# Kernel tuning notes

Measured on AMD Instinct MI355X. Metric: run time of the kernel, lower is better.

The kernel has to match this reference:

```python
import jax, jax.numpy as jnp
import numpy as np

N, E, FE = 20000, 160000, 500000
IN, HC, HEADS = 128, 64, 4
HEADC = HC // HEADS          # 16
DV = HEADC                   # 16
KHOP = 3
NUM_T = 128
OUT = 1
CST = 1e-5


def _lin(key, fan_in, fan_out):
    kw, kb = jax.random.split(key)
    s = 1.0 / np.sqrt(fan_in)
    W = jax.random.uniform(kw, (fan_in, fan_out), minval=-s, maxval=s, dtype=jnp.float32)
    b = jax.random.uniform(kb, (fan_out,), minval=-s, maxval=s, dtype=jnp.float32)
    return W, b


def setup_inputs() -> dict:
    key = jax.random.key(0)
    ks = jax.random.split(key, 16)
    x = jax.random.normal(ks[0], (N, IN), dtype=jnp.float32)
    edge_index = jax.random.randint(ks[1], (2, E), 0, N, dtype=jnp.int32)
    full_edge_index = jax.random.randint(ks[2], (2, FE), 0, N, dtype=jnp.int32)
    time_steps = jax.random.randint(ks[3], (N,), 0, NUM_T, dtype=jnp.int32)
    Wi, bi = _lin(ks[4], IN, HC)
    Wt1, bt1 = _lin(ks[5], HC, 4 * HC)
    Wt2, bt2 = _lin(ks[6], 4 * HC, HC)
    WQ, bQ = _lin(ks[7], HC, HEADS * HEADC)
    WK, bK = _lin(ks[8], HC, HEADS * HEADC)
    WV, bV = _lin(ks[9], HC, HEADS * DV)
    Wo, bo = _lin(ks[10], HEADS * DV, DV)
    hopwise = jnp.ones((KHOP + 1,), dtype=jnp.float32)
    headwise = jnp.zeros((HEADS, KHOP), dtype=jnp.float32)
    Wf1, bf1 = _lin(ks[11], 2 * DV, DV)
    Wf2, bf2 = _lin(ks[12], DV, OUT)
    return dict(x=x, edge_index=edge_index, full_edge_index=full_edge_index,
                time_steps=time_steps, Wi=Wi, bi=bi, Wt1=Wt1, bt1=bt1,
                Wt2=Wt2, bt2=bt2, WQ=WQ, bQ=bQ, WK=WK, bK=bK, WV=WV, bV=bV,
                Wo=Wo, bo=bo, hopwise=hopwise, headwise=headwise,
                Wf1=Wf1, bf1=bf1, Wf2=Wf2, bf2=bf2)


def _sin_emb(t, dim, num_steps, rescale=4000.0):
    # Sinusoidal timestep embedding rescaled by num_steps (diffusion style).
    t = t.astype(jnp.float32) * (rescale / num_steps)
    half = dim // 2
    freqs = jnp.exp(-jnp.log(10000.0) / (half - 1) * jnp.arange(half, dtype=jnp.float32))
    args = t[:, None] * freqs[None, :]
    return jnp.concatenate([jnp.sin(args), jnp.cos(args)], axis=-1)


def reference(x, edge_index, full_edge_index, time_steps,
              Wi, bi, Wt1, bt1, Wt2, bt2, WQ, bQ, WK, bK, WV, bV,
              Wo, bo, hopwise, headwise, Wf1, bf1, Wf2, bf2):
    n = x.shape[0]
    row, col = edge_index[0], edge_index[1]

    # random-walk norm: deg over destination (col), norm gathered at source (row)
    deg = jax.ops.segment_sum(jnp.ones_like(col, dtype=x.dtype), col, num_segments=n)
    deg_inv = jnp.where(deg > 0, 1.0 / deg, 0.0)
    norm = deg_inv[row]                                   # [E]

    t_emb = _sin_emb(time_steps, HC, NUM_T)               # [N, HC]
    t_emb = jax.nn.silu(t_emb @ Wt1 + bt1) @ Wt2 + bt2    # [N, HC]

    h = jax.nn.relu(x @ Wi + bi + t_emb)                  # [N, HC]

    Q = (1.0 + jax.nn.elu(h @ WQ + bQ)).reshape(n, HEADS, HEADC)
    Kf = (1.0 + jax.nn.elu(h @ WK + bK)).reshape(n, HEADS, HEADC)
    V = (h @ WV + bV).reshape(n, HEADS, DV)

    M = jnp.einsum('nhi,nhj->nhij', Kf, V)                # [N, H, hc, dv]
    hidden = V * hopwise[0]
    layerwise = jax.nn.softmax(headwise, axis=0)          # softmax over heads

    for hop in range(KHOP):
        # gather-scale-scatter message passing (random walk propagation)
        M = jax.ops.segment_sum(M[row] * norm[:, None, None, None], col, num_segments=n)
        Kf = jax.ops.segment_sum(Kf[row] * norm[:, None, None], col, num_segments=n)
        H = jnp.einsum('nhi,nhij->nhj', Q, M)             # [N, H, dv]
        C = jnp.einsum('nhi,nhi->nh', Q, Kf)[..., None] + CST
        gamma = hopwise[hop + 1] * layerwise[:, hop][:, None]   # [H, 1]
        hidden = hidden + gamma * (H / C)

    # multi_concat output projection
    hidden = hidden.reshape(n, HEADS * DV) @ Wo + bo      # [N, DV]

    src, dst = full_edge_index[0], full_edge_index[1]
    he = jnp.concatenate([hidden[src], hidden[dst]], axis=-1)  # [FE, 2*DV]
    edge_logits = jax.nn.silu(he @ Wf1 + bf1) @ Wf2 + bf2      # [FE, OUT]
    return edge_logits, hidden
```

## Files before the change

### kernel.cpp

```cpp
#include <hip/hip_runtime.h>
#include <math.h>


#define HC 64
#define HEADS 4
#define KHOP 3
#define NUM_T 128
#define MSZ 1024
#define SLOTS 64
#define CST 1e-5f

typedef float f32x2 __attribute__((ext_vector_type(2)));

__device__ __forceinline__ float bf2f(unsigned short s) { return __uint_as_float(((unsigned int)s) << 16); }
__device__ __forceinline__ float bfu_lo(unsigned int u) { return __uint_as_float(u << 16); }
__device__ __forceinline__ float bfu_hi(unsigned int u) { return __uint_as_float(u & 0xffff0000u); }
__device__ __forceinline__ unsigned short f2bf(float f) {
    unsigned int u = __float_as_uint(f);
    u = (u + 0x7fffu + ((u >> 16) & 1u)) >> 16;
    return (unsigned short)u;
}
__device__ __forceinline__ unsigned int pack4fp8(float a, float b, float c, float d) {
    int r = __builtin_amdgcn_cvt_pk_fp8_f32(a, b, 0, false);
    r = __builtin_amdgcn_cvt_pk_fp8_f32(c, d, r, true);
    return (unsigned int)r;
}

__global__ void k_fill(const int* __restrict__ row, const int* __restrict__ col,
                       int* __restrict__ cnt, int* __restrict__ csr, int E) {
    int e = blockIdx.x * 256 + threadIdx.x;
    if (e >= E) return;
    int c = col[e];
    int r = row[e];
    int k = atomicAdd(&cnt[c], 1);
    if (k < SLOTS) csr[c * SLOTS + k] = r;
}

__global__ __launch_bounds__(256) void k_misc(
    const float* __restrict__ Wt1, const float* __restrict__ bt1,
    const float* __restrict__ Wt2, const float* __restrict__ bt2,
    const float* __restrict__ hopwise, const float* __restrict__ headwise,
    const int* __restrict__ cnt,
    float* __restrict__ gamma, float* __restrict__ table,
    float* __restrict__ inv_deg, int n) {
    if (blockIdx.x >= NUM_T) {
        int i = (blockIdx.x - NUM_T) * 256 + threadIdx.x;
        if (i < n) {
            int d = cnt[i];
            inv_deg[i] = (d > 0) ? 1.0f / (float)min(d, SLOTS) : 0.0f;
        }
        return;
    }
    if (blockIdx.x == 0 && threadIdx.x == 0) {
        for (int k = 0; k < KHOP; k++) {
            float m = -1e30f;
            for (int h2 = 0; h2 < HEADS; h2++) m = fmaxf(m, headwise[h2 * KHOP + k]);
            float ex[HEADS]; float s = 0.f;
            for (int h2 = 0; h2 < HEADS; h2++) { ex[h2] = expf(headwise[h2 * KHOP + k] - m); s += ex[h2]; }
            for (int h2 = 0; h2 < HEADS; h2++) gamma[k * HEADS + h2] = hopwise[k + 1] * ex[h2] / s;
        }
    }
    int t = threadIdx.x;
    int tval = blockIdx.x;
    __shared__ float emb_s[64];
    __shared__ float z1_s[256];
    __shared__ float ps_s[4][64];
    if (t < 64) {
        float tt = (float)tval * 31.25f;
        float e;
        if (t < 32) e = sinf(tt * expf(-0.2971077539347156f * (float)t));
        else        e = cosf(tt * expf(-0.2971077539347156f * (float)(t - 32)));
        emb_s[t] = e;
    }
    __syncthreads();
    {
        float acc = bt1[t];
        #pragma unroll 8
        for (int i = 0; i < 64; i++) acc += emb_s[i] * Wt1[i * 256 + t];
        z1_s[t] = acc / (1.f + expf(-acc));
    }
    __syncthreads();
    {
        int j = t & 63, p = t >> 6;
        float acc = 0.f;
        #pragma unroll 8
        for (int i = 0; i < 64; i++) acc += z1_s[p * 64 + i] * Wt2[(p * 64 + i) * 64 + j];
        ps_s[p][j] = acc;
    }
    __syncthreads();
    if (t < 64)
        table[tval * 64 + t] = ps_s[0][t] + ps_s[1][t] + ps_s[2][t] + ps_s[3][t] + bt2[t];
}

__global__ __launch_bounds__(256) void k_node(
    const float* __restrict__ x, const int* __restrict__ time_steps,
    const float* __restrict__ temb, const float* __restrict__ Wi,
    const float* __restrict__ bi,
    const float* __restrict__ WQ, const float* __restrict__ bQ,
    const float* __restrict__ WK, const float* __restrict__ bK,
    const float* __restrict__ WV, const float* __restrict__ bV,
    const float* __restrict__ hopwise, const float* __restrict__ inv_deg,
    float* __restrict__ Q, unsigned short* __restrict__ Kf0,
    unsigned short* __restrict__ Vbuf, float* __restrict__ hidden, int n) {
    __shared__ float xs[16][128];
    __shared__ float hs[16][64];
    int j = threadIdx.x & 63;
    int slot = threadIdx.x >> 6;
    int nbase = blockIdx.x * 16;
    int nvalid = min(16, n - nbase);
    const float4* xg = (const float4*)(x + (size_t)nbase * 128);
    float4* xs4 = (float4*)&xs[0][0];
    for (int idx = threadIdx.x; idx < nvalid * 32; idx += 256) xs4[idx] = xg[idx];
    __syncthreads();
    int nl = slot * 4;
    {
        float acc[4];
        #pragma unroll
        for (int k = 0; k < 4; k++) acc[k] = 0.f;
        #pragma unroll 8
        for (int i = 0; i < 128; i++) {
            float w = Wi[i * 64 + j];
            #pragma unroll
            for (int k = 0; k < 4; k++) acc[k] += xs[nl + k][i] * w;
        }
        float bj = bi[j];
        #pragma unroll
        for (int k = 0; k < 4; k++) {
            int node = nbase + nl + k;
            float te = (node < n) ? temb[time_steps[node] * 64 + j] : 0.f;
            hs[nl + k][j] = fmaxf(acc[k] + bj + te, 0.f);
        }
    }
    __syncthreads();
    float aq[4], ak[4], av[4];
    #pragma unroll
    for (int k = 0; k < 4; k++) { aq[k] = bQ[j]; ak[k] = bK[j]; av[k] = bV[j]; }
    #pragma unroll 4
    for (int i = 0; i < 64; i++) {
        float wq = WQ[i * 64 + j], wk = WK[i * 64 + j], wv = WV[i * 64 + j];
        #pragma unroll
        for (int k = 0; k < 4; k++) {
            float hv = hs[nl + k][i];
            aq[k] += hv * wq; ak[k] += hv * wk; av[k] += hv * wv;
        }
    }
    float h0 = hopwise[0];
    #pragma unroll
    for (int k = 0; k < 4; k++) {
        int node = nbase + nl + k;
        if (node < n) {
            float q  = 1.f + ((aq[k] > 0.f) ? aq[k] : (expf(aq[k]) - 1.f));
            float kf = 1.f + ((ak[k] > 0.f) ? ak[k] : (expf(ak[k]) - 1.f));
            float inv = inv_deg[node];
            Q[(size_t)node * 64 + j] = q;
            Kf0[(size_t)node * 64 + j] = f2bf(kf * inv);
            Vbuf[(size_t)node * 64 + j] = f2bf(av[k]);
            hidden[(size_t)node * 64 + j] = av[k] * h0;
        }
    }
}

template<int MODE>
__global__ __launch_bounds__(128) void k_hop(
    const unsigned char* __restrict__ Mold, const unsigned short* __restrict__ Kfold,
    const unsigned short* __restrict__ Vbuf,
    const int* __restrict__ cnt, const int* __restrict__ csr,
    const float* __restrict__ inv_deg, const float* __restrict__ Q,
    const float* __restrict__ gamma,
    unsigned char* __restrict__ Mnew, unsigned short* __restrict__ Kfnew,
    float* __restrict__ hidden, int hop, int write_out,
    const float* __restrict__ Wo, const float* __restrict__ bo,
    const float* __restrict__ Wf1, float* __restrict__ out16,
    float* __restrict__ Pbuf, int n) {
    constexpr int DEPTH = (MODE == 0) ? 4 : 8;
    int lane = threadIdx.x & 63;
    int node = blockIdx.x * 2 + (threadIdx.x >> 6);
    if (node >= n) return;
    int grp = lane >> 4;
    int deg = min(cnt[node], SLOTS);
    int sidx = csr[(size_t)node * SLOTS + lane];
    float qv = Q[(size_t)node * 64 + lane];
    size_t hoff = (size_t)node * 64 + lane;
    float hid_in = hidden[hoff];
    int degU = __builtin_amdgcn_readfirstlane(deg);
    float acc[16];
    #pragma unroll
    for (int t = 0; t < 16; t++) acc[t] = 0.f;
    float kacc = 0.f;

    int d = 0;
    for (; d + DEPTH <= degU; d += DEPTH) {
        unsigned short kraw[DEPTH];
        uint4 m0[DEPTH], m1[DEPTH];
        #pragma unroll
        for (int t = 0; t < DEPTH; t++) {
            int s = __builtin_amdgcn_readlane(sidx, d + t);
            kraw[t] = Kfold[(size_t)s * 64 + lane];
            if constexpr (MODE == 0) {
                const uint4* vp = (const uint4*)((const unsigned char*)Vbuf + (size_t)s * 128 + grp * 32);
                m0[t] = vp[0]; m1[t] = vp[1];
            } else {
                m0[t] = *(const uint4*)(Mold + (size_t)s * MSZ + lane * 16);
            }
        }
        #pragma unroll
        for (int t = 0; t < DEPTH; t++) {
            float kf = bf2f(kraw[t]);
            kacc += kf;
            if constexpr (MODE == 0) {
                acc[0]  = fmaf(kf, bfu_lo(m0[t].x), acc[0]);
                acc[1]  = fmaf(kf, bfu_hi(m0[t].x), acc[1]);
                acc[2]  = fmaf(kf, bfu_lo(m0[t].y), acc[2]);
                acc[3]  = fmaf(kf, bfu_hi(m0[t].y), acc[3]);
                acc[4]  = fmaf(kf, bfu_lo(m0[t].z), acc[4]);
                acc[5]  = fmaf(kf, bfu_hi(m0[t].z), acc[5]);
                acc[6]  = fmaf(kf, bfu_lo(m0[t].w), acc[6]);
                acc[7]  = fmaf(kf, bfu_hi(m0[t].w), acc[7]);
                acc[8]  = fmaf(kf, bfu_lo(m1[t].x), acc[8]);
                acc[9]  = fmaf(kf, bfu_hi(m1[t].x), acc[9]);
                acc[10] = fmaf(kf, bfu_lo(m1[t].y), acc[10]);
                acc[11] = fmaf(kf, bfu_hi(m1[t].y), acc[11]);
                acc[12] = fmaf(kf, bfu_lo(m1[t].z), acc[12]);
                acc[13] = fmaf(kf, bfu_hi(m1[t].z), acc[13]);
                acc[14] = fmaf(kf, bfu_lo(m1[t].w), acc[14]);
                acc[15] = fmaf(kf, bfu_hi(m1[t].w), acc[15]);
            } else {
                f32x2 p;
                p = __builtin_amdgcn_cvt_pk_f32_fp8((int)m0[t].x, false); acc[0]  += p.x; acc[1]  += p.y;
                p = __builtin_amdgcn_cvt_pk_f32_fp8((int)m0[t].x, true);  acc[2]  += p.x; acc[3]  += p.y;
                p = __builtin_amdgcn_cvt_pk_f32_fp8((int)m0[t].y, false); acc[4]  += p.x; acc[5]  += p.y;
                p = __builtin_amdgcn_cvt_pk_f32_fp8((int)m0[t].y, true);  acc[6]  += p.x; acc[7]  += p.y;
                p = __builtin_amdgcn_cvt_pk_f32_fp8((int)m0[t].z, false); acc[8]  += p.x; acc[9]  += p.y;
                p = __builtin_amdgcn_cvt_pk_f32_fp8((int)m0[t].z, true);  acc[10] += p.x; acc[11] += p.y;
                p = __builtin_amdgcn_cvt_pk_f32_fp8((int)m0[t].w, false); acc[12] += p.x; acc[13] += p.y;
                p = __builtin_amdgcn_cvt_pk_f32_fp8((int)m0[t].w, true);  acc[14] += p.x; acc[15] += p.y;
            }
        }
    }
    if (d < degU) {
        int rem = degU - d;
        unsigned short kraw[DEPTH];
        uint4 m0[DEPTH], m1[DEPTH];
        #pragma unroll
        for (int t = 0; t < DEPTH - 1; t++) {
            if (t < rem) {
                int s = __builtin_amdgcn_readlane(sidx, d + t);
                kraw[t] = Kfold[(size_t)s * 64 + lane];
                if constexpr (MODE == 0) {
                    const uint4* vp = (const uint4*)((const unsigned char*)Vbuf + (size_t)s * 128 + grp * 32);
                    m0[t] = vp[0]; m1[t] = vp[1];
                } else {
                    m0[t] = *(const uint4*)(Mold + (size_t)s * MSZ + lane * 16);
                }
            }
        }
        #pragma unroll
        for (int t = 0; t < DEPTH - 1; t++) {
            if (t < rem) {
                float kf = bf2f(kraw[t]);
                kacc += kf;
                if constexpr (MODE == 0) {
                    acc[0]  = fmaf(kf, bfu_lo(m0[t].x), acc[0]);
                    acc[1]  = fmaf(kf, bfu_hi(m0[t].x), acc[1]);
                    acc[2]  = fmaf(kf, bfu_lo(m0[t].y), acc[2]);
                    acc[3]  = fmaf(kf, bfu_hi(m0[t].y), acc[3]);
                    acc[4]  = fmaf(kf, bfu_lo(m0[t].z), acc[4]);
                    acc[5]  = fmaf(kf, bfu_hi(m0[t].z), acc[5]);
                    acc[6]  = fmaf(kf, bfu_lo(m0[t].w), acc[6]);
                    acc[7]  = fmaf(kf, bfu_hi(m0[t].w), acc[7]);
                    acc[8]  = fmaf(kf, bfu_lo(m1[t].x), acc[8]);
                    acc[9]  = fmaf(kf, bfu_hi(m1[t].x), acc[9]);
                    acc[10] = fmaf(kf, bfu_lo(m1[t].y), acc[10]);
                    acc[11] = fmaf(kf, bfu_hi(m1[t].y), acc[11]);
                    acc[12] = fmaf(kf, bfu_lo(m1[t].z), acc[12]);
                    acc[13] = fmaf(kf, bfu_hi(m1[t].z), acc[13]);
                    acc[14] = fmaf(kf, bfu_lo(m1[t].w), acc[14]);
                    acc[15] = fmaf(kf, bfu_hi(m1[t].w), acc[15]);
                } else {
                    f32x2 p;
                    p = __builtin_amdgcn_cvt_pk_f32_fp8((int)m0[t].x, false); acc[0]  += p.x; acc[1]  += p.y;
                    p = __builtin_amdgcn_cvt_pk_f32_fp8((int)m0[t].x, true);  acc[2]  += p.x; acc[3]  += p.y;
                    p = __builtin_amdgcn_cvt_pk_f32_fp8((int)m0[t].y, false); acc[4]  += p.x; acc[5]  += p.y;
                    p = __builtin_amdgcn_cvt_pk_f32_fp8((int)m0[t].y, true);  acc[6]  += p.x; acc[7]  += p.y;
                    p = __builtin_amdgcn_cvt_pk_f32_fp8((int)m0[t].z, false); acc[8]  += p.x; acc[9]  += p.y;
                    p = __builtin_amdgcn_cvt_pk_f32_fp8((int)m0[t].z, true);  acc[10] += p.x; acc[11] += p.y;
                    p = __builtin_amdgcn_cvt_pk_f32_fp8((int)m0[t].w, false); acc[12] += p.x; acc[13] += p.y;
                    p = __builtin_amdgcn_cvt_pk_f32_fp8((int)m0[t].w, true);  acc[14] += p.x; acc[15] += p.y;
                }
            }
        }
    }

    if (write_out) {
        float inv = inv_deg[node];
        uint4 st;
        st.x = pack4fp8(acc[0] * inv,  acc[1] * inv,  acc[2] * inv,  acc[3] * inv);
        st.y = pack4fp8(acc[4] * inv,  acc[5] * inv,  acc[6] * inv,  acc[7] * inv);
        st.z = pack4fp8(acc[8] * inv,  acc[9] * inv,  acc[10] * inv, acc[11] * inv);
        st.w = pack4fp8(acc[12] * inv, acc[13] * inv, acc[14] * inv, acc[15] * inv);
        *(uint4*)(Mnew + (size_t)node * MSZ + lane * 16) = st;
        Kfnew[(size_t)node * 64 + lane] = f2bf(kacc * inv);
    }

    float c = qv * kacc;
    c += __shfl_xor(c, 1); c += __shfl_xor(c, 2); c += __shfl_xor(c, 4); c += __shfl_xor(c, 8);

    float w0[16];
    #pragma unroll
    for (int t = 0; t < 16; t++) w0[t] = qv * acc[t];
    float w1r[8];
    #pragma unroll
    for (int t = 0; t < 8; t++) {
        float a = w0[2 * t], b = w0[2 * t + 1];
        float mine = (lane & 1) ? b : a, th = (lane & 1) ? a : b;
        w1r[t] = mine + __shfl_xor(th, 1);
    }
    float w2r[4];
    #pragma unroll
    for (int t = 0; t < 4; t++) {
        float a = w1r[2 * t], b = w1r[2 * t + 1];
        float mine = (lane & 2) ? b : a, th = (lane & 2) ? a : b;
        w2r[t] = mine + __shfl_xor(th, 2);
    }
    float w3r[2];
    #pragma unroll
    for (int t = 0; t < 2; t++) {
        float a = w2r[2 * t], b = w2r[2 * t + 1];
        float mine = (lane & 4) ? b : a, th = (lane & 4) ? a : b;
        w3r[t] = mine + __shfl_xor(th, 4);
    }
    float Hv;
    {
        float a = w3r[0], b = w3r[1];
        float mine = (lane & 8) ? b : a, th = (lane & 8) ? a : b;
        Hv = mine + __shfl_xor(th, 8);
    }

    float g = gamma[hop * HEADS + grp];
    float contrib = g * Hv / (c + CST);
    if (write_out) {
        hidden[hoff] = hid_in + contrib;
    } else {
        float hid = hid_in + contrib;
        const float4* wop = (const float4*)(Wo + lane * 16);
        float4 wo0 = wop[0], wo1 = wop[1], wo2 = wop[2], wo3 = wop[3];
        float v[16];
        v[0] = hid * wo0.x;  v[1] = hid * wo0.y;  v[2] = hid * wo0.z;  v[3] = hid * wo0.w;
        v[4] = hid * wo1.x;  v[5] = hid * wo1.y;  v[6] = hid * wo1.z;  v[7] = hid * wo1.w;
        v[8] = hid * wo2.x;  v[9] = hid * wo2.y;  v[10] = hid * wo2.z; v[11] = hid * wo2.w;
        v[12] = hid * wo3.x; v[13] = hid * wo3.y; v[14] = hid * wo3.z; v[15] = hid * wo3.w;
        #pragma unroll
        for (int m = 32; m >= 1; m >>= 1) {
            #pragma unroll
            for (int o = 0; o < 16; o++) v[o] += __shfl_xor(v[o], m);
        }
        #pragma unroll
        for (int o = 0; o < 16; o++) v[o] += bo[o];
        if (lane == 0) {
            float4* op = (float4*)(out16 + (size_t)node * 16);
            op[0] = make_float4(v[0],  v[1],  v[2],  v[3]);
            op[1] = make_float4(v[4],  v[5],  v[6],  v[7]);
            op[2] = make_float4(v[8],  v[9],  v[10], v[11]);
            op[3] = make_float4(v[12], v[13], v[14], v[15]);
        }
        if (lane < 32) {
            int o = lane & 15, half = lane >> 4;
            const float* wf = Wf1 + (size_t)(half * 16) * 16 + o;
            float p = 0.f;
            #pragma unroll
            for (int i = 0; i < 16; i++) p += v[i] * wf[i * 16];
            Pbuf[(size_t)node * 32 + lane] = p;
        }
    }
}

__global__ __launch_bounds__(256) void k_edge(
    const int* __restrict__ src, const int* __restrict__ dst,
    const float* __restrict__ Pbuf,
    const float* __restrict__ bf1, const float* __restrict__ Wf2,
    const float* __restrict__ bf2,
    float* __restrict__ out, int fe) {
    __shared__ float b1[16];
    __shared__ float w2[16];
    __shared__ float b2s;
    int t = threadIdx.x;
    if (t < 16) { b1[t] = bf1[t]; w2[t] = Wf2[t]; }
    if (t == 0) b2s = bf2[0];
    __syncthreads();
    int e = blockIdx.x * 256 + t;
    if (e >= fe) return;
    int s = src[e], d = dst[e];
    const float4* p1 = (const float4*)(Pbuf + (size_t)s * 32);
    const float4* p2 = (const float4*)(Pbuf + (size_t)d * 32 + 16);
    float z[16];
    #pragma unroll
    for (int q = 0; q < 4; q++) {
        float4 a = p1[q]; float4 b = p2[q];
        z[q * 4 + 0] = a.x + b.x; z[q * 4 + 1] = a.y + b.y;
        z[q * 4 + 2] = a.z + b.z; z[q * 4 + 3] = a.w + b.w;
    }
    float acc = b2s;
    #pragma unroll
    for (int o = 0; o < 16; o++) {
        float zz = z[o] + b1[o];
        zz = zz / (1.f + expf(-zz));
// ... 17 lines not shown
    const float* bt2 = (const float*)d_in[9];
    const float* WQ  = (const float*)d_in[10];
    const float* bQ  = (const float*)d_in[11];
    const float* WK  = (const float*)d_in[12];
    const float* bK  = (const float*)d_in[13];
    const float* WV  = (const float*)d_in[14];
    const float* bV  = (const float*)d_in[15];
    const float* Wo  = (const float*)d_in[16];
    const float* bo  = (const float*)d_in[17];
    const float* hopwise  = (const float*)d_in[18];
    const float* headwise = (const float*)d_in[19];
    const float* Wf1 = (const float*)d_in[20];
    const float* bf1 = (const float*)d_in[21];
    const float* Wf2 = (const float*)d_in[22];
    const float* bf2 = (const float*)d_in[23];

    const int N  = in_sizes[3];
    const int E  = in_sizes[1] / 2;
    const int FE = in_sizes[2] / 2;
    const int* row = eidx;
    const int* col = eidx + E;
    const int* fsrc = feidx;
    const int* fdst = feidx + FE;

    char* ws = (char*)d_ws;
    size_t off = 0;
    auto alloc = [&](size_t bytes) -> char* {
        char* p = ws + off;
        off = (off + bytes + 255) & ~(size_t)255;
        return p;
    };
    float* gamma     = (float*)alloc(KHOP * HEADS * sizeof(float));
    int*   cnt       = (int*)alloc((size_t)N * 4);
    int*   csr       = (int*)alloc((size_t)N * SLOTS * 4);
    float* inv_deg   = (float*)alloc((size_t)N * 4);
    float* temb      = (float*)alloc((size_t)NUM_T * HC * 4);
    float* Qbuf      = (float*)alloc((size_t)N * HC * 4);
    unsigned short* Kf0  = (unsigned short*)alloc((size_t)N * HC * 2);
    unsigned short* Kf_a = (unsigned short*)alloc((size_t)N * HC * 2);
    unsigned short* Kf_b = (unsigned short*)alloc((size_t)N * HC * 2);
    unsigned short* Vbuf = (unsigned short*)alloc((size_t)N * HC * 2);
    float* hidden    = (float*)alloc((size_t)N * HC * 4);
    unsigned char* M_a = (unsigned char*)alloc((size_t)N * MSZ);
    unsigned char* M_b = (unsigned char*)alloc((size_t)N * MSZ);
    float* Pbuf      = (float*)alloc((size_t)N * 32 * 4);
    (void)ws_size;

    float* out_edges = (float*)d_out;
    float* out_hid16 = (float*)d_out + FE;

    const int miscBlocks = NUM_T + (N + 255) / 256;
    const int hopBlocks = (N + 1) / 2;

    (void)hipMemsetAsync(cnt, 0, (size_t)N * 4, stream);
    k_fill<<<(E + 255) / 256, 256, 0, stream>>>(row, col, cnt, csr, E);
    k_misc<<<miscBlocks, 256, 0, stream>>>(Wt1, bt1, Wt2, bt2, hopwise, headwise,
                                           cnt, gamma, temb, inv_deg, N);
    k_node<<<(N + 15) / 16, 256, 0, stream>>>(x, tsteps, temb, Wi, bi,
                                              WQ, bQ, WK, bK, WV, bV, hopwise, inv_deg,
                                              Qbuf, Kf0, Vbuf, hidden, N);
    k_hop<0><<<hopBlocks, 128, 0, stream>>>(nullptr, Kf0, Vbuf, cnt, csr, inv_deg, Qbuf, gamma,
                                            M_a, Kf_a, hidden, 0, 1, Wo, bo, Wf1, out_hid16, Pbuf, N);
    k_hop<1><<<hopBlocks, 128, 0, stream>>>(M_a, Kf_a, nullptr, cnt, csr, inv_deg, Qbuf, gamma,
                                            M_b, Kf_b, hidden, 1, 1, Wo, bo, Wf1, out_hid16, Pbuf, N);
    k_hop<1><<<hopBlocks, 128, 0, stream>>>(M_b, Kf_b, nullptr, cnt, csr, inv_deg, Qbuf, gamma,
                                            M_a, Kf_a, hidden, 2, 0, Wo, bo, Wf1, out_hid16, Pbuf, N);
    k_edge<<<(FE + 255) / 256, 256, 0, stream>>>(fsrc, fdst, Pbuf, bf1, Wf2, bf2,
                                                 out_edges, FE);
}
```

Baseline: 253.9 us.

## Split hop kernel across 8 M-slices per node group and defer combine to new kernel

Result: slower. 351.9 us (+38.6%).

```diff
diff --git a/kernel.cpp b/kernel.cpp
--- a/kernel.cpp
+++ b/kernel.cpp
@@ -99,9 +99,9 @@
     const float* __restrict__ WQ, const float* __restrict__ bQ,
     const float* __restrict__ WK, const float* __restrict__ bK,
     const float* __restrict__ WV, const float* __restrict__ bV,
-    const float* __restrict__ hopwise, const float* __restrict__ inv_deg,
+    const float* __restrict__ inv_deg,
     float* __restrict__ Q, unsigned short* __restrict__ Kf0,
-    unsigned short* __restrict__ Vbuf, float* __restrict__ hidden, int n) {
+    unsigned short* __restrict__ Vbuf, int n) {
     __shared__ float xs[16][128];
     __shared__ float hs[16][64];
     int j = threadIdx.x & 63;
@@ -144,7 +144,6 @@
             aq[k] += hv * wq; ak[k] += hv * wk; av[k] += hv * wv;
         }
     }
-    float h0 = hopwise[0];
     #pragma unroll
     for (int k = 0; k < 4; k++) {
         int node = nbase + nl + k;
@@ -155,222 +154,173 @@
             Q[(size_t)node * 64 + j] = q;
             Kf0[(size_t)node * 64 + j] = f2bf(kf * inv);
             Vbuf[(size_t)node * 64 + j] = f2bf(av[k]);
-            hidden[(size_t)node * 64 + j] = av[k] * h0;
         }
     }
 }
 
 template<int MODE>
-__global__ __launch_bounds__(128) void k_hop(
+__global__ __launch_bounds__(256) void k_hop(
     const unsigned char* __restrict__ Mold, const unsigned short* __restrict__ Kfold,
-    const unsigned short* __restrict__ Vbuf,
+    const unsigned short* __restrict__ Vb,
     const int* __restrict__ cnt, const int* __restrict__ csr,
     const float* __restrict__ inv_deg, const float* __restrict__ Q,
-    const float* __restrict__ gamma,
     unsigned char* __restrict__ Mnew, unsigned short* __restrict__ Kfnew,
-    float* __restrict__ hidden, int hop, int write_out,
-    const float* __restrict__ Wo, const float* __restrict__ bo,
-    const float* __restrict__ Wf1, float* __restrict__ out16,
-    float* __restrict__ Pbuf, int n) {
-    constexpr int DEPTH = (MODE == 0) ? 4 : 8;
+    float* __restrict__ Hp, float* __restrict__ Cp,
+    int hop, int write_out, int n) {
     int lane = threadIdx.x & 63;
-    int node = blockIdx.x * 2 + (threadIdx.x >> 6);
-    if (node >= n) return;
-    int grp = lane >> 4;
-    int deg = min(cnt[node], SLOTS);
-    int sidx = csr[(size_t)node * SLOTS + lane];
-    float qv = Q[(size_t)node * 64 + lane];
-    size_t hoff = (size_t)node * 64 + lane;
-    float hid_in = hidden[hoff];
-    int degU = __builtin_amdgcn_readfirstlane(deg);
-    float acc[16];
-    #pragma unroll
-    for (int t = 0; t < 16; t++) acc[t] = 0.f;
+    int wv   = threadIdx.x >> 6;
+    int slice = blockIdx.x & 7;
+    int ngrp  = blockIdx.x >> 3;
+    int ell   = lane & 15;
+    int gbase = lane & 48;
+    int node  = ngrp * 16 + wv * 4 + (lane >> 4);
+    int h = slice >> 1, ib = (slice & 1) * 8;
+    int i_loc = ell >> 1, jh = ell & 1;
+    bool valid = node < n;
+    int deg = 0; int s0 = 0, s1 = 0, s2 = 0, s3 = 0; float qv = 0.f;
+    if (valid) {
+        deg = min(__builtin_nontemporal_load(cnt + node), SLOTS);
+        const int* cb = csr + (size_t)node * SLOTS;
+        s0 = __builtin_nontemporal_load(cb + ell);
+        s1 = __builtin_nontemporal_load(cb + 16 + ell);
+        s2 = __builtin_nontemporal_load(cb + 32 + ell);
+        s3 = __builtin_nontemporal_load(cb + 48 + ell);
+        qv = Q[(size_t)node * 64 + h * 16 + ib + i_loc];
+    }
+    int dm = max(deg, __shfl_xor(deg, 16));
+    dm = max(dm, __shfl_xor(dm, 32));
+    int degU = __builtin_amdgcn_readfirstlane(dm);
+
+    float acc[8];
+    #pragma unroll
+    for (int t = 0; t < 8; t++) acc[t] = 0.f;
     float kacc = 0.f;
 
-    int d = 0;
-    for (; d + DEPTH <= degU; d += DEPTH) {
-        unsigned short kraw[DEPTH];
-        uint4 m0[DEPTH], m1[DEPTH];
-        #pragma unroll
-        for (int t = 0; t < DEPTH; t++) {
-            int s = __builtin_amdgcn_readlane(sidx, d + t);
-            kraw[t] = Kfold[(size_t)s * 64 + lane];
-            if constexpr (MODE == 0) {
-                const uint4* vp = (const uint4*)((const unsigned char*)Vbuf + (size_t)s * 128 + grp * 32);
-                m0[t] = vp[0]; m1[t] = vp[1];
-            } else {
-                m0[t] = *(const uint4*)(Mold + (size_t)s * MSZ + lane * 16);
-            }
-        }
-        #pragma unroll
-        for (int t = 0; t < DEPTH; t++) {
-            float kf = bf2f(kraw[t]);
-            kacc += kf;
-            if constexpr (MODE == 0) {
-                acc[0]  = fmaf(kf, bfu_lo(m0[t].x), acc[0]);
-                acc[1]  = fmaf(kf, bfu_hi(m0[t].x), acc[1]);
-                acc[2]  = fmaf(kf, bfu_lo(m0[t].y), acc[2]);
-                acc[3]  = fmaf(kf, bfu_hi(m0[t].y), acc[3]);
-                acc[4]  = fmaf(kf, bfu_lo(m0[t].z), acc[4]);
-                acc[5]  = fmaf(kf, bfu_hi(m0[t].z), acc[5]);
-                acc[6]  = fmaf(kf, bfu_lo(m0[t].w), acc[6]);
-                acc[7]  = fmaf(kf, bfu_hi(m0[t].w), acc[7]);
-                acc[8]  = fmaf(kf, bfu_lo(m1[t].x), acc[8]);
-                acc[9]  = fmaf(kf, bfu_hi(m1[t].x), acc[9]);
-                acc[10] = fmaf(kf, bfu_lo(m1[t].y), acc[10]);
-                acc[11] = fmaf(kf, bfu_hi(m1[t].y), acc[11]);
-                acc[12] = fmaf(kf, bfu_lo(m1[t].z), acc[12]);
-                acc[13] = fmaf(kf, bfu_hi(m1[t].z), acc[13]);
-                acc[14] = fmaf(kf, bfu_lo(m1[t].w), acc[14]);
-                acc[15] = fmaf(kf, bfu_hi(m1[t].w), acc[15]);
-            } else {
-                f32x2 p;
-                p = __builtin_amdgcn_cvt_pk_f32_fp8((int)m0[t].x, false); acc[0]  += p.x; acc[1]  += p.y;
-                p = __builtin_amdgcn_cvt_pk_f32_fp8((int)m0[t].x, true);  acc[2]  += p.x; acc[3]  += p.y;
-                p = __builtin_amdgcn_cvt_pk_f32_fp8((int)m0[t].y, false); acc[4]  += p.x; acc[5]  += p.y;
-                p = __builtin_amdgcn_cvt_pk_f32_fp8((int)m0[t].y, true);  acc[6]  += p.x; acc[7]  += p.y;
-                p = __builtin_amdgcn_cvt_pk_f32_fp8((int)m0[t].z, false); acc[8]  += p.x; acc[9]  += p.y;
-                p = __builtin_amdgcn_cvt_pk_f32_fp8((int)m0[t].z, true);  acc[10] += p.x; acc[11] += p.y;
-                p = __builtin_amdgcn_cvt_pk_f32_fp8((int)m0[t].w, false); acc[12] += p.x; acc[13] += p.y;
-                p = __builtin_amdgcn_cvt_pk_f32_fp8((int)m0[t].w, true);  acc[14] += p.x; acc[15] += p.y;
-            }
-        }
-    }
-    if (d < degU) {
-        int rem = degU - d;
-        unsigned short kraw[DEPTH];
-        uint4 m0[DEPTH], m1[DEPTH];
-        #pragma unroll
-        for (int t = 0; t < DEPTH - 1; t++) {
-            if (t < rem) {
-                int s = __builtin_amdgcn_readlane(sidx, d + t);
-                kraw[t] = Kfold[(size_t)s * 64 + lane];
-                if constexpr (MODE == 0) {
-                    const uint4* vp = (const uint4*)((const unsigned char*)Vbuf + (size_t)s * 128 + grp * 32);
-                    m0[t] = vp[0]; m1[t] = vp[1];
-                } else {
-                    m0[t] = *(const uint4*)(Mold + (size_t)s * MSZ + lane * 16);
+    constexpr int SUB = (MODE == 0) ? 8 : 16;
+    #pragma unroll
+    for (int blk = 0; blk < 4; blk++) {
+        if (blk * 16 >= degU) break;
+        int sreg = (blk == 0) ? s0 : (blk == 1) ? s1 : (blk == 2) ? s2 : s3;
+        #pragma unroll
+        for (int sb = 0; sb < 16 / SUB; sb++) {
+            unsigned int kr[SUB];
+            uint2 mv[(MODE == 1) ? SUB : 1];
+            uint4 vvv[(MODE == 0) ? SUB : 1];
+            #pragma unroll
+            for (int t = 0; t < SUB; t++) {
+                int sl = sb * SUB + t;
+                int q = blk * 16 + sl;
+                int sv = __shfl(sreg, gbase + sl);
+                kr[t] = 0u;
+                if constexpr (MODE == 0) { vvv[t] = make_uint4(0, 0, 0, 0); }
+                else { mv[t].x = 0u; mv[t].y = 0u; }
+                if (q < deg) {
+                    kr[t] = (unsigned int)Kfold[(size_t)sv * 64 + h * 16 + ib + i_loc];
+                    if constexpr (MODE == 0)
+                        vvv[t] = *(const uint4*)(Vb + (size_t)sv * 64 + h * 16 + jh * 8);
+                    else
+                        mv[t] = *(const uint2*)(Mold + (size_t)sv * MSZ + slice * 128 + ell * 8);
                 }
             }
-        }
-        #pragma unroll
-        for (int t = 0; t < DEPTH - 1; t++) {
-            if (t < rem) {
-                float kf = bf2f(kraw[t]);
+            #pragma unroll
+            for (int t = 0; t < SUB; t++) {
+                float kf = bf2f((unsigned short)kr[t]);
                 kacc += kf;
                 if constexpr (MODE == 0) {
-                    acc[0]  = fmaf(kf, bfu_lo(m0[t].x), acc[0]);
-                    acc[1]  = fmaf(kf, bfu_hi(m0[t].x), acc[1]);
-                    acc[2]  = fmaf(kf, bfu_lo(m0[t].y), acc[2]);
-                    acc[3]  = fmaf(kf, bfu_hi(m0[t].y), acc[3]);
-                    acc[4]  = fmaf(kf, bfu_lo(m0[t].z), acc[4]);
-                    acc[5]  = fmaf(kf, bfu_hi(m0[t].z), acc[5]);
-                    acc[6]  = fmaf(kf, bfu_lo(m0[t].w), acc[6]);
-                    acc[7]  = fmaf(kf, bfu_hi(m0[t].w), acc[7]);
-                    acc[8]  = fmaf(kf, bfu_lo(m1[t].x), acc[8]);
-                    acc[9]  = fmaf(kf, bfu_hi(m1[t].x), acc[9]);
-                    acc[10] = fmaf(kf, bfu_lo(m1[t].y), acc[10]);
-                    acc[11] = fmaf(kf, bfu_hi(m1[t].y), acc[11]);
-                    acc[12] = fmaf(kf, bfu_lo(m1[t].z), acc[12]);
-                    acc[13] = fmaf(kf, bfu_hi(m1[t].z), acc[13]);
-                    acc[14] = fmaf(kf, bfu_lo(m1[t].w), acc[14]);
-                    acc[15] = fmaf(kf, bfu_hi(m1[t].w), acc[15]);
+                    acc[0] += kf * bfu_lo(vvv[t].x); acc[1] += kf * bfu_hi(vvv[t].x);
+                    acc[2] += kf * bfu_lo(vvv[t].y); acc[3] += kf * bfu_hi(vvv[t].y);
+                    acc[4] += kf * bfu_lo(vvv[t].z); acc[5] += kf * bfu_hi(vvv[t].z);
+                    acc[6] += kf * bfu_lo(vvv[t].w); acc[7] += kf * bfu_hi(vvv[t].w);
                 } else {
                     f32x2 p;
-                    p = __builtin_amdgcn_cvt_pk_f32_fp8((int)m0[t].x, false); acc[0]  += p.x; acc[1]  += p.y;
-                    p = __builtin_amdgcn_cvt_pk_f32_fp8((int)m0[t].x, true);  acc[2]  += p.x; acc[3]  += p.y;
-                    p = __builtin_amdgcn_cvt_pk_f32_fp8((int)m0[t].y, false); acc[4]  += p.x; acc[5]  += p.y;
-                    p = __builtin_amdgcn_cvt_pk_f32_fp8((int)m0[t].y, true);  acc[6]  += p.x; acc[7]  += p.y;
-                    p = __builtin_amdgcn_cvt_pk_f32_fp8((int)m0[t].z, false); acc[8]  += p.x; acc[9]  += p.y;
-                    p = __builtin_amdgcn_cvt_pk_f32_fp8((int)m0[t].z, true);  acc[10] += p.x; acc[11] += p.y;
-                    p = __builtin_amdgcn_cvt_pk_f32_fp8((int)m0[t].w, false); acc[12] += p.x; acc[13] += p.y;
-                    p = __builtin_amdgcn_cvt_pk_f32_fp8((int)m0[t].w, true);  acc[14] += p.x; acc[15] += p.y;
+                    p = __builtin_amdgcn_cvt_pk_f32_fp8((int)mv[t].x, false); acc[0] += p.x; acc[1] += p.y;
+                    p = __builtin_amdgcn_cvt_pk_f32_fp8((int)mv[t].x, true);  acc[2] += p.x; acc[3] += p.y;
+                    p = __builtin_amdgcn_cvt_pk_f32_fp8((int)mv[t].y, false); acc[4] += p.x; acc[5] += p.y;
+                    p = __builtin_amdgcn_cvt_pk_f32_fp8((int)mv[t].y, true);  acc[6] += p.x; acc[7] += p.y;
                 }
             }
         }
     }
 
-    if (write_out) {
+    if (valid && write_out) {
         float inv = inv_deg[node];
-        uint4 st;
-        st.x = pack4fp8(acc[0] * inv,  acc[1] * inv,  acc[2] * inv,  acc[3] * inv);
-        st.y = pack4fp8(acc[4] * inv,  acc[5] * inv,  acc[6] * inv,  acc[7] * inv);
-        st.z = pack4fp8(acc[8] * inv,  acc[9] * inv,  acc[10] * inv, acc[11] * inv);
-        st.w = pack4fp8(acc[12] * inv, acc[13] * inv, acc[14] * inv, acc[15] * inv);
-        *(uint4*)(Mnew + (size_t)node * MSZ + lane * 16) = st;
-        Kfnew[(size_t)node * 64 + lane] = f2bf(kacc * inv);
-    }
-
-    float c = qv * kacc;
-    c += __shfl_xor(c, 1); c += __shfl_xor(c, 2); c += __shfl_xor(c, 4); c += __shfl_xor(c, 8);
-
-    float w0[16];
-    #pragma unroll
-    for (int t = 0; t < 16; t++) w0[t] = qv * acc[t];
-    float w1r[8];
-    #pragma unroll
-    for (int t = 0; t < 8; t++) {
-        float a = w0[2 * t], b = w0[2 * t + 1];
-        float mine = (lane & 1) ? b : a, th = (lane & 1) ? a : b;
-        w1r[t] = mine + __shfl_xor(th, 1);
-    }
-    float w2r[4];
-    #pragma unroll
-    for (int t = 0; t < 4; t++) {
-        float a = w1r[2 * t], b = w1r[2 * t + 1];
-        float mine = (lane & 2) ? b : a, th = (lane & 2) ? a : b;
-        w2r[t] = mine + __shfl_xor(th, 2);
-    }
-    float w3r[2];
-    #pragma unroll
-    for (int t = 0; t < 2; t++) {
-        float a = w2r[2 * t], b = w2r[2 * t + 1];
-        float mine = (lane & 4) ? b : a, th = (lane & 4) ? a : b;
-        w3r[t] = mine + __shfl_xor(th, 4);
-    }
-    float Hv;
-    {
-        float a = w3r[0], b = w3r[1];
-        float mine = (lane & 8) ? b : a, th = (lane & 8) ? a : b;
-        Hv = mine + __shfl_xor(th, 8);
-    }
-
-    float g = gamma[hop * HEADS + grp];
-    float contrib = g * Hv / (c + CST);
-    if (write_out) {
-        hidden[hoff] = hid_in + contrib;
-    } else {
-        float hid = hid_in + contrib;
-        const float4* wop = (const float4*)(Wo + lane * 16);
-        float4 wo0 = wop[0], wo1 = wop[1], wo2 = wop[2], wo3 = wop[3];
-        float v[16];
-        v[0] = hid * wo0.x;  v[1] = hid * wo0.y;  v[2] = hid * wo0.z;  v[3] = hid * wo0.w;
-        v[4] = hid * wo1.x;  v[5] = hid * wo1.y;  v[6] = hid * wo1.z;  v[7] = hid * wo1.w;
-        v[8] = hid * wo2.x;  v[9] = hid * wo2.y;  v[10] = hid * wo2.z; v[11] = hid * wo2.w;
-        v[12] = hid * wo3.x; v[13] = hid * wo3.y; v[14] = hid * wo3.z; v[15] = hid * wo3.w;
-        #pragma unroll
-        for (int m = 32; m >= 1; m >>= 1) {
-            #pragma unroll
-            for (int o = 0; o < 16; o++) v[o] += __shfl_xor(v[o], m);
-        }
-        #pragma unroll
-        for (int o = 0; o < 16; o++) v[o] += bo[o];
-        if (lane == 0) {
-            float4* op = (float4*)(out16 + (size_t)node * 16);
-            op[0] = make_float4(v[0],  v[1],  v[2],  v[3]);
-            op[1] = make_float4(v[4],  v[5],  v[6],  v[7]);
-            op[2] = make_float4(v[8],  v[9],  v[10], v[11]);
-            op[3] = make_float4(v[12], v[13], v[14], v[15]);
-        }
-        if (lane < 32) {
-            int o = lane & 15, half = lane >> 4;
-            const float* wf = Wf1 + (size_t)(half * 16) * 16 + o;
-            float p = 0.f;
-            #pragma unroll
-            for (int i = 0; i < 16; i++) p += v[i] * wf[i * 16];
-            Pbuf[(size_t)node * 32 + lane] = p;
-        }
+        uint2 st;
+        st.x = pack4fp8(acc[0] * inv, acc[1] * inv, acc[2] * inv, acc[3] * inv);
+        st.y = pack4fp8(acc[4] * inv, acc[5] * inv, acc[6] * inv, acc[7] * inv);
+        *(uint2*)(Mnew + (size_t)node * MSZ + slice * 128 + ell * 8) = st;
+        if (jh == 0) Kfnew[(size_t)node * 64 + h * 16 + ib + i_loc] = f2bf(kacc * inv);
+    }
+
+    float w[8];
+    #pragma unroll
+    for (int k = 0; k < 8; k++) w[k] = qv * acc[k];
+    #pragma unroll
+    for (int m = 2; m <= 8; m <<= 1) {
+        #pragma unroll
+        for (int k = 0; k < 8; k++) w[k] += __shfl_xor(w[k], m);
+    }
+    float ck = (jh == 0) ? qv * kacc : 0.f;
+    ck += __shfl_xor(ck, 1); ck += __shfl_xor(ck, 2);
+    ck += __shfl_xor(ck, 4); ck += __shfl_xor(ck, 8);
+
+    if (valid) {
+        float* hpb = Hp + ((size_t)hop * n + node) * 128 + slice * 16;
+        if (ell < 2) {
+            *(float4*)(hpb + jh * 8)     = make_float4(w[0], w[1], w[2], w[3]);
+            *(float4*)(hpb + jh * 8 + 4) = make_float4(w[4], w[5], w[6], w[7]);
+        }
+        if (ell == 0) Cp[((size_t)hop * n + node) * 8 + slice] = ck;
+    }
+}
+
+__global__ __launch_bounds__(256) void k_comb(
+    const unsigned short* __restrict__ Vb,
+    const float* __restrict__ Hp, const float* __restrict__ Cp,
+    const float* __restrict__ gamma, const float* __restrict__ hopwise,
+    const float* __restrict__ Wo, const float* __restrict__ bo,
+    const float* __restrict__ Wf1,
+    float* __restrict__ out16, float* __restrict__ Pbuf, int n) {
+    int lane = threadIdx.x & 63;
+    int node = blockIdx.x * 4 + (threadIdx.x >> 6);
+    if (node >= n) return;
+    int h = lane >> 4, j = lane & 15;
+    float hid = hopwise[0] * bf2f(Vb[(size_t)node * 64 + lane]);
+    #pragma unroll
+    for (int hop = 0; hop < KHOP; hop++) {
+        const float* hpb = Hp + ((size_t)hop * n + node) * 128;
+        const float* cpb = Cp + ((size_t)hop * n + node) * 8;
+        float Hs = hpb[(2 * h) * 16 + j] + hpb[(2 * h + 1) * 16 + j];
+        float Cs = cpb[2 * h] + cpb[2 * h + 1] + CST;
+        hid += gamma[hop * HEADS + h] * Hs / Cs;
+    }
+    const float4* wop = (const float4*)(Wo + lane * 16);
+    float4 wo0 = wop[0], wo1 = wop[1], wo2 = wop[2], wo3 = wop[3];
+    float v[16];
+    v[0] = hid * wo0.x;  v[1] = hid * wo0.y;  v[2] = hid * wo0.z;  v[3] = hid * wo0.w;
+    v[4] = hid * wo1.x;  v[5] = hid * wo1.y;  v[6] = hid * wo1.z;  v[7] = hid * wo1.w;
+    v[8] = hid * wo2.x;  v[9] = hid * wo2.y;  v[10] = hid * wo2.z; v[11] = hid * wo2.w;
+    v[12] = hid * wo3.x; v[13] = hid * wo3.y; v[14] = hid * wo3.z; v[15] = hid * wo3.w;
+    #pragma unroll
+    for (int m = 32; m >= 1; m >>= 1) {
+        #pragma unroll
+        for (int o = 0; o < 16; o++) v[o] += __shfl_xor(v[o], m);
+    }
+    #pragma unroll
+    for (int o = 0; o < 16; o++) v[o] += bo[o];
+    if (lane == 0) {
+        float4* op = (float4*)(out16 + (size_t)node * 16);
+        op[0] = make_float4(v[0],  v[1],  v[2],  v[3]);
+        op[1] = make_float4(v[4],  v[5],  v[6],  v[7]);
+        op[2] = make_float4(v[8],  v[9],  v[10], v[11]);
+        op[3] = make_float4(v[12], v[13], v[14], v[15]);
+    }
+    if (lane < 32) {
+        int o = lane & 15, half = lane >> 4;
+        const float* wf = Wf1 + (size_t)(half * 16) * 16 + o;
+        float p = 0.f;
+        #pragma unroll
+        for (int i = 0; i < 16; i++) p += v[i] * wf[i * 16];
+        Pbuf[(size_t)node * 32 + lane] = p;
     }
 }
 
@@ -462,9 +412,10 @@
     unsigned short* Kf_a = (unsigned short*)alloc((size_t)N * HC * 2);
     unsigned short* Kf_b = (unsigned short*)alloc((size_t)N * HC * 2);
     unsigned short* Vbuf = (unsigned short*)alloc((size_t)N * HC * 2);
-    float* hidden    = (float*)alloc((size_t)N * HC * 4);
     unsigned char* M_a = (unsigned char*)alloc((size_t)N * MSZ);
     unsigned char* M_b = (unsigned char*)alloc((size_t)N * MSZ);
+    float* Hp        = (float*)alloc((size_t)KHOP * N * 128 * 4);
+    float* Cp        = (float*)alloc((size_t)KHOP * N * 8 * 4);
     float* Pbuf      = (float*)alloc((size_t)N * 32 * 4);
     (void)ws_size;
 
@@ -472,21 +423,23 @@
     float* out_hid16 = (float*)d_out + FE;
 
     const int miscBlocks = NUM_T + (N + 255) / 256;
-    const int hopBlocks = (N + 1) / 2;
+    const int hopBlocks = 8 * ((N + 15) / 16);
 
     (void)hipMemsetAsync(cnt, 0, (size_t)N * 4, stream);
     k_fill<<<(E + 255) / 256, 256, 0, stream>>>(row, col, cnt, csr, E);
     k_misc<<<miscBlocks, 256, 0, stream>>>(Wt1, bt1, Wt2, bt2, hopwise, headwise,
                                            cnt, gamma, temb, inv_deg, N);
     k_node<<<(N + 15) / 16, 256, 0, stream>>>(x, tsteps, temb, Wi, bi,
-                                              WQ, bQ, WK, bK, WV, bV, hopwise, inv_deg,
-                                              Qbuf, Kf0, Vbuf, hidden, N);
-    k_hop<0><<<hopBlocks, 128, 0, stream>>>(nullptr, Kf0, Vbuf, cnt, csr, inv_deg, Qbuf, gamma,
-                                            M_a, Kf_a, hidden, 0, 1, Wo, bo, Wf1, out_hid16, Pbuf, N);
-    k_hop<1><<<hopBlocks, 128, 0, stream>>>(M_a, Kf_a, nullptr, cnt, csr, inv_deg, Qbuf, gamma,
-                                            M_b, Kf_b, hidden, 1, 1, Wo, bo, Wf1, out_hid16, Pbuf, N);
-    k_hop<1><<<hopBlocks, 128, 0, stream>>>(M_b, Kf_b, nullptr, cnt, csr, inv_deg, Qbuf, gamma,
-                                            M_a, Kf_a, hidden, 2, 0, Wo, bo, Wf1, out_hid16, Pbuf, N);
+                                              WQ, bQ, WK, bK, WV, bV, inv_deg,
+                                              Qbuf, Kf0, Vbuf, N);
+    k_hop<0><<<hopBlocks, 256, 0, stream>>>(nullptr, Kf0, Vbuf, cnt, csr, inv_deg, Qbuf,
+                                            M_a, Kf_a, Hp, Cp, 0, 1, N);
+    k_hop<1><<<hopBlocks, 256, 0, stream>>>(M_a, Kf_a, nullptr, cnt, csr, inv_deg, Qbuf,
+                                            M_b, Kf_b, Hp, Cp, 1, 1, N);
+    k_hop<1><<<hopBlocks, 256, 0, stream>>>(M_b, Kf_b, nullptr, cnt, csr, inv_deg, Qbuf,
+                                            M_a, Kf_a, Hp, Cp, 2, 0, N);
+    k_comb<<<(N + 3) / 4, 256, 0, stream>>>(Vbuf, Hp, Cp, gamma, hopwise,
+                                            Wo, bo, Wf1, out_hid16, Pbuf, N);
     k_edge<<<(FE + 255) / 256, 256, 0, stream>>>(fsrc, fdst, Pbuf, bf1, Wf2, bf2,
                                                  out_edges, FE);
 }
```

## Replace final hop gather of M with push-style Q·M scatter via atomics

Applied to the files above, without the earlier changes.

Result: slower. 297.6 us (+17.2%).

```diff
diff --git a/kernel.cpp b/kernel.cpp
--- a/kernel.cpp
+++ b/kernel.cpp
@@ -11,6 +11,7 @@
 #define CST 1e-5f
 
 typedef float f32x2 __attribute__((ext_vector_type(2)));
+typedef unsigned int u32x4 __attribute__((ext_vector_type(4)));
 
 __device__ __forceinline__ float bf2f(unsigned short s) { return __uint_as_float(((unsigned int)s) << 16); }
 __device__ __forceinline__ float bfu_lo(unsigned int u) { return __uint_as_float(u << 16); }
@@ -27,13 +28,16 @@
 }
 
 __global__ void k_fill(const int* __restrict__ row, const int* __restrict__ col,
-                       int* __restrict__ cnt, int* __restrict__ csr, int E) {
+                       int* __restrict__ cnt, int* __restrict__ csr,
+                       int* __restrict__ ocnt, int* __restrict__ ocsr, int E) {
     int e = blockIdx.x * 256 + threadIdx.x;
     if (e >= E) return;
     int c = col[e];
     int r = row[e];
     int k = atomicAdd(&cnt[c], 1);
     if (k < SLOTS) csr[c * SLOTS + k] = r;
+    int k2 = atomicAdd(&ocnt[r], 1);
+    if (k2 < SLOTS) ocsr[r * SLOTS + k2] = c;
 }
 
 __global__ __launch_bounds__(256) void k_misc(
@@ -100,7 +104,8 @@
     const float* __restrict__ WK, const float* __restrict__ bK,
     const float* __restrict__ WV, const float* __restrict__ bV,
     const float* __restrict__ hopwise, const float* __restrict__ inv_deg,
-    float* __restrict__ Q, unsigned short* __restrict__ Kf0,
+    float* __restrict__ Q, unsigned short* __restrict__ Qbf,
+    unsigned short* __restrict__ Kf0,
     unsigned short* __restrict__ Vbuf, float* __restrict__ hidden, int n) {
     __shared__ float xs[16][128];
     __shared__ float hs[16][64];
@@ -153,6 +158,7 @@
             float kf = 1.f + ((ak[k] > 0.f) ? ak[k] : (expf(ak[k]) - 1.f));
             float inv = inv_deg[node];
             Q[(size_t)node * 64 + j] = q;
+            Qbf[(size_t)node * 64 + j] = f2bf(q);
             Kf0[(size_t)node * 64 + j] = f2bf(kf * inv);
             Vbuf[(size_t)node * 64 + j] = f2bf(av[k]);
             hidden[(size_t)node * 64 + j] = av[k] * h0;
@@ -168,10 +174,7 @@
     const float* __restrict__ inv_deg, const float* __restrict__ Q,
     const float* __restrict__ gamma,
     unsigned char* __restrict__ Mnew, unsigned short* __restrict__ Kfnew,
-    float* __restrict__ hidden, int hop, int write_out,
-    const float* __restrict__ Wo, const float* __restrict__ bo,
-    const float* __restrict__ Wf1, float* __restrict__ out16,
-    float* __restrict__ Pbuf, int n) {
+    float* __restrict__ hidden, int hop, int n) {
     constexpr int DEPTH = (MODE == 0) ? 4 : 8;
     int lane = threadIdx.x & 63;
     int node = blockIdx.x * 2 + (threadIdx.x >> 6);
@@ -291,7 +294,7 @@
         }
     }
 
-    if (write_out) {
+    {
         float inv = inv_deg[node];
         uint4 st;
         st.x = pack4fp8(acc[0] * inv,  acc[1] * inv,  acc[2] * inv,  acc[3] * inv);
@@ -337,40 +340,131 @@
     }
 
     float g = gamma[hop * HEADS + grp];
-    float contrib = g * Hv / (c + CST);
-    if (write_out) {
-        hidden[hoff] = hid_in + contrib;
-    } else {
-        float hid = hid_in + contrib;
-        const float4* wop = (const float4*)(Wo + lane * 16);
-        float4 wo0 = wop[0], wo1 = wop[1], wo2 = wop[2], wo3 = wop[3];
-        float v[16];
-        v[0] = hid * wo0.x;  v[1] = hid * wo0.y;  v[2] = hid * wo0.z;  v[3] = hid * wo0.w;
-        v[4] = hid * wo1.x;  v[5] = hid * wo1.y;  v[6] = hid * wo1.z;  v[7] = hid * wo1.w;
-        v[8] = hid * wo2.x;  v[9] = hid * wo2.y;  v[10] = hid * wo2.z; v[11] = hid * wo2.w;
-        v[12] = hid * wo3.x; v[13] = hid * wo3.y; v[14] = hid * wo3.z; v[15] = hid * wo3.w;
-        #pragma unroll
-        for (int m = 32; m >= 1; m >>= 1) {
-            #pragma unroll
-            for (int o = 0; o < 16; o++) v[o] += __shfl_xor(v[o], m);
-        }
-        #pragma unroll
-        for (int o = 0; o < 16; o++) v[o] += bo[o];
-        if (lane == 0) {
-            float4* op = (float4*)(out16 + (size_t)node * 16);
-            op[0] = make_float4(v[0],  v[1],  v[2],  v[3]);
-            op[1] = make_float4(v[4],  v[5],  v[6],  v[7]);
-            op[2] = make_float4(v[8],  v[9],  v[10], v[11]);
-            op[3] = make_float4(v[12], v[13], v[14], v[15]);
-        }
-        if (lane < 32) {
-            int o = lane & 15, half = lane >> 4;
-            const float* wf = Wf1 + (size_t)(half * 16) * 16 + o;
-            float p = 0.f;
-            #pragma unroll
-            for (int i = 0; i < 16; i++) p += v[i] * wf[i * 16];
-            Pbuf[(size_t)node * 32 + lane] = p;
-        }
+    hidden[hoff] = hid_in + g * Hv / (c + CST);
+}
+
+__global__ __launch_bounds__(128) void k_push(
+    const unsigned char* __restrict__ Mb, const unsigned short* __restrict__ Kfb,
+    const int* __restrict__ ocnt, const int* __restrict__ ocsr,
+    const unsigned short* __restrict__ Qbf,
+    float* __restrict__ Hp, float* __restrict__ Cp, int n) {
+    int lane = threadIdx.x & 63;
+    int node = blockIdx.x * 2 + (threadIdx.x >> 6);
+    if (node >= n) return;
+    int od = min(ocnt[node], SLOTS);
+    int odU = __builtin_amdgcn_readfirstlane(od);
+    if (odU == 0) return;
+    int dsts = ocsr[(size_t)node * SLOTS + lane];
+    u32x4 mraw = __builtin_nontemporal_load((const u32x4*)(Mb + (size_t)node * MSZ + lane * 16));
+    float kf = bf2f(__builtin_nontemporal_load(Kfb + (size_t)node * 64 + lane));
+    float mrow[16];
+    {
+        f32x2 p;
+        p = __builtin_amdgcn_cvt_pk_f32_fp8((int)mraw.x, false); mrow[0]  = p.x; mrow[1]  = p.y;
+        p = __builtin_amdgcn_cvt_pk_f32_fp8((int)mraw.x, true);  mrow[2]  = p.x; mrow[3]  = p.y;
+        p = __builtin_amdgcn_cvt_pk_f32_fp8((int)mraw.y, false); mrow[4]  = p.x; mrow[5]  = p.y;
+        p = __builtin_amdgcn_cvt_pk_f32_fp8((int)mraw.y, true);  mrow[6]  = p.x; mrow[7]  = p.y;
+        p = __builtin_amdgcn_cvt_pk_f32_fp8((int)mraw.z, false); mrow[8]  = p.x; mrow[9]  = p.y;
+        p = __builtin_amdgcn_cvt_pk_f32_fp8((int)mraw.z, true);  mrow[10] = p.x; mrow[11] = p.y;
+        p = __builtin_amdgcn_cvt_pk_f32_fp8((int)mraw.w, false); mrow[12] = p.x; mrow[13] = p.y;
+        p = __builtin_amdgcn_cvt_pk_f32_fp8((int)mraw.w, true);  mrow[14] = p.x; mrow[15] = p.y;
+    }
+    for (int base = 0; base < odU; base += 8) {
+        int rem = odU - base;
+        float qv[8]; int dd[8];
+        #pragma unroll
+        for (int t = 0; t < 8; t++) {
+            if (t < rem) {
+                dd[t] = __builtin_amdgcn_readlane(dsts, base + t);
+                qv[t] = bf2f(Qbf[(size_t)dd[t] * 64 + lane]);
+            }
+        }
+        #pragma unroll
+        for (int t = 0; t < 8; t++) {
+            if (t < rem) {
+                float q = qv[t];
+                float c = q * kf;
+                c += __shfl_xor(c, 1); c += __shfl_xor(c, 2);
+                c += __shfl_xor(c, 4); c += __shfl_xor(c, 8);
+                float w0[16];
+                #pragma unroll
+                for (int k = 0; k < 16; k++) w0[k] = q * mrow[k];
+                float w1r[8];
+                #pragma unroll
+                for (int k = 0; k < 8; k++) {
+                    float a = w0[2 * k], b = w0[2 * k + 1];
+                    float mine = (lane & 1) ? b : a, th = (lane & 1) ? a : b;
+                    w1r[k] = mine + __shfl_xor(th, 1);
+                }
+                float w2r[4];
+                #pragma unroll
+                for (int k = 0; k < 4; k++) {
+                    float a = w1r[2 * k], b = w1r[2 * k + 1];
+                    float mine = (lane & 2) ? b : a, th = (lane & 2) ? a : b;
+                    w2r[k] = mine + __shfl_xor(th, 2);
+                }
+                float w3r[2];
+                #pragma unroll
+                for (int k = 0; k < 2; k++) {
+                    float a = w2r[2 * k], b = w2r[2 * k + 1];
+                    float mine = (lane & 4) ? b : a, th = (lane & 4) ? a : b;
+                    w3r[k] = mine + __shfl_xor(th, 4);
+                }
+                float Hv;
+                {
+                    float a = w3r[0], b = w3r[1];
+                    float mine = (lane & 8) ? b : a, th = (lane & 8) ? a : b;
+                    Hv = mine + __shfl_xor(th, 8);
+                }
+                atomicAdd(Hp + (size_t)dd[t] * 64 + lane, Hv);
+                if ((lane & 15) == 0) atomicAdd(Cp + (size_t)dd[t] * 4 + (lane >> 4), c);
+            }
+        }
+    }
+}
+
+__global__ __launch_bounds__(256) void k_comb(
+    const float* __restrict__ hidden,
+    const float* __restrict__ Hp, const float* __restrict__ Cp,
+    const float* __restrict__ gamma,
+    const float* __restrict__ Wo, const float* __restrict__ bo,
+    const float* __restrict__ Wf1,
+    float* __restrict__ out16, float* __restrict__ Pbuf, int n) {
+    int lane = threadIdx.x & 63;
+    int node = blockIdx.x * 4 + (threadIdx.x >> 6);
+    if (node >= n) return;
+    int h = lane >> 4;
+    float H = Hp[(size_t)node * 64 + lane];
+    float C = Cp[(size_t)node * 4 + h] + CST;
+    float hid = hidden[(size_t)node * 64 + lane] + gamma[2 * HEADS + h] * H / C;
+    const float4* wop = (const float4*)(Wo + lane * 16);
+    float4 wo0 = wop[0], wo1 = wop[1], wo2 = wop[2], wo3 = wop[3];
+    float v[16];
+    v[0] = hid * wo0.x;  v[1] = hid * wo0.y;  v[2] = hid * wo0.z;  v[3] = hid * wo0.w;
+    v[4] = hid * wo1.x;  v[5] = hid * wo1.y;  v[6] = hid * wo1.z;  v[7] = hid * wo1.w;
+    v[8] = hid * wo2.x;  v[9] = hid * wo2.y;  v[10] = hid * wo2.z; v[11] = hid * wo2.w;
+    v[12] = hid * wo3.x; v[13] = hid * wo3.y; v[14] = hid * wo3.z; v[15] = hid * wo3.w;
+    #pragma unroll
+    for (int m = 32; m >= 1; m >>= 1) {
+        #pragma unroll
+        for (int o = 0; o < 16; o++) v[o] += __shfl_xor(v[o], m);
+    }
+    #pragma unroll
+    for (int o = 0; o < 16; o++) v[o] += bo[o];
+    if (lane == 0) {
+        float4* op = (float4*)(out16 + (size_t)node * 16);
+        op[0] = make_float4(v[0],  v[1],  v[2],  v[3]);
+        op[1] = make_float4(v[4],  v[5],  v[6],  v[7]);
+        op[2] = make_float4(v[8],  v[9],  v[10], v[11]);
+        op[3] = make_float4(v[12], v[13], v[14], v[15]);
+    }
+    if (lane < 32) {
+        int o = lane & 15, half = lane >> 4;
+        const float* wf = Wf1 + (size_t)(half * 16) * 16 + o;
+        float p = 0.f;
+        #pragma unroll
+        for (int i = 0; i < 16; i++) p += v[i] * wf[i * 16];
+        Pbuf[(size_t)node * 32 + lane] = p;
     }
 }
 
@@ -454,10 +548,16 @@
     };
     float* gamma     = (float*)alloc(KHOP * HEADS * sizeof(float));
     int*   cnt       = (int*)alloc((size_t)N * 4);
+    int*   ocnt      = (int*)alloc((size_t)N * 4);
+    float* Cp        = (float*)alloc((size_t)N * 4 * 4);
+    float* Hp        = (float*)alloc((size_t)N * 64 * 4);
+    size_t zlen      = (size_t)((char*)(Hp + (size_t)N * 64) - (char*)cnt);
     int*   csr       = (int*)alloc((size_t)N * SLOTS * 4);
+    int*   ocsr      = (int*)alloc((size_t)N * SLOTS * 4);
     float* inv_deg   = (float*)alloc((size_t)N * 4);
     float* temb      = (float*)alloc((size_t)NUM_T * HC * 4);
     float* Qbuf      = (float*)alloc((size_t)N * HC * 4);
+    unsigned short* Qbf  = (unsigned short*)alloc((size_t)N * HC * 2);
     unsigned short* Kf0  = (unsigned short*)alloc((size_t)N * HC * 2);
     unsigned short* Kf_a = (unsigned short*)alloc((size_t)N * HC * 2);
     unsigned short* Kf_b = (unsigned short*)alloc((size_t)N * HC * 2);
@@ -474,19 +574,20 @@
     const int miscBlocks = NUM_T + (N + 255) / 256;
     const int hopBlocks = (N + 1) / 2;
 
-    (void)hipMemsetAsync(cnt, 0, (size_t)N * 4, stream);
-    k_fill<<<(E + 255) / 256, 256, 0, stream>>>(row, col, cnt, csr, E);
+    (void)hipMemsetAsync(cnt, 0, zlen, stream);
+    k_fill<<<(E + 255) / 256, 256, 0, stream>>>(row, col, cnt, csr, ocnt, ocsr, E);
     k_misc<<<miscBlocks, 256, 0, stream>>>(Wt1, bt1, Wt2, bt2, hopwise, headwise,
                                            cnt, gamma, temb, inv_deg, N);
     k_node<<<(N + 15) / 16, 256, 0, stream>>>(x, tsteps, temb, Wi, bi,
                                               WQ, bQ, WK, bK, WV, bV, hopwise, inv_deg,
-                                              Qbuf, Kf0, Vbuf, hidden, N);
-    k_hop<0><<<hopBlocks, 128, 0, stream>>>(nullptr, Kf0, Vbuf, cnt, csr, inv_deg, Qbuf, gamma,
-                                            M_a, Kf_a, hidden, 0, 1, Wo, bo, Wf1, out_hid16, Pbuf, N);
-    k_hop<1><<<hopBlocks, 128, 0, stream>>>(M_a, Kf_a, nullptr, cnt, csr, inv_deg, Qbuf, gamma,
-                                            M_b, Kf_b, hidden, 1, 1, Wo, bo, Wf1, out_hid16, Pbuf, N);
-    k_hop<1><<<hopBlocks, 128, 0, stream>>>(M_b, Kf_b, nullptr, cnt, csr, inv_deg, Qbuf, gamma,
-                                            M_a, Kf_a, hidden, 2, 0, Wo, bo, Wf1, out_hid16, Pbuf, N);
+                                              Qbuf, Qbf, Kf0, Vbuf, hidden, N);
+    k_hop<0><<<hopBlocks, 128, 0, stream>>>(nullptr, Kf0, Vbuf, cnt, csr, inv_deg, Qbuf,
+                                            gamma, M_a, Kf_a, hidden, 0, N);
+    k_hop<1><<<hopBlocks, 128, 0, stream>>>(M_a, Kf_a, nullptr, cnt, csr, inv_deg, Qbuf,
+                                            gamma, M_b, Kf_b, hidden, 1, N);
+    k_push<<<hopBlocks, 128, 0, stream>>>(M_b, Kf_b, ocnt, ocsr, Qbf, Hp, Cp, N);
+    k_comb<<<(N + 3) / 4, 256, 0, stream>>>(hidden, Hp, Cp, gamma, Wo, bo, Wf1,
+                                            out_hid16, Pbuf, N);
     k_edge<<<(FE + 255) / 256, 256, 0, stream>>>(fsrc, fdst, Pbuf, bf1, Wf2, bf2,
                                                  out_edges, FE);
 }
```
